# Optimization experiments

Measured on AMD Instinct MI355X. Metric: run time of the kernel, lower is better.

The kernel has to match this reference:

```python
import jax, jax.numpy as jnp
import numpy as np

VOCAB, EMB, HID, B, T = 50000, 300, 150, 256, 512

def _lstm_params(key, in_dim, hid):
    k1, k2, k3, k4 = jax.random.split(key, 4)
    s = 1.0 / np.sqrt(hid)
    return (jax.random.uniform(k1, (4 * hid, in_dim), minval=-s, maxval=s),
            jax.random.uniform(k2, (4 * hid, hid), minval=-s, maxval=s),
            jax.random.uniform(k3, (4 * hid,), minval=-s, maxval=s),
            jax.random.uniform(k4, (4 * hid,), minval=-s, maxval=s))

def setup_inputs() -> dict:
    key = jax.random.key(0)
    ks = jax.random.split(key, 16)
    emb = jax.random.normal(ks[0], (VOCAB, EMB), dtype=jnp.float32)
    emb = emb.at[0].set(0.0)  # padding_idx=0
    x = jax.random.randint(ks[1], (B, T), 0, VOCAB, dtype=jnp.int64)
    lengths = jax.random.randint(ks[2], (B,), 1, T + 1, dtype=jnp.int64)
    inp = {"x": x, "lengths": lengths, "emb": emb}
    in_dims = [EMB, HID, HID, HID]  # lstm1 layers 0,1 ; lstm2 layers 0,1
    for l in range(4):
        Wih, Whh, bih, bhh = _lstm_params(ks[3 + l], in_dims[l], HID)
        inp[f"Wih{l}"], inp[f"Whh{l}"], inp[f"bih{l}"], inp[f"bhh{l}"] = Wih, Whh, bih, bhh
    s = 1.0 / np.sqrt(HID)
    inp["fc1_w"] = jax.random.uniform(ks[8], (HID, HID), minval=-s, maxval=s)
    inp["fc1_b"] = jax.random.uniform(ks[9], (HID,), minval=-s, maxval=s)
    inp["fc2_w"] = jax.random.uniform(ks[10], (1, HID), minval=-s, maxval=s)
    inp["fc2_b"] = jax.random.uniform(ks[11], (1,), minval=-s, maxval=s)
    return inp

def _lstm_layer(x_seq, lengths, Wih, Whh, bih, bhh):
    # x_seq: [B, T, D]. Packed-sequence semantics: state updated only while t < length;
    # padded output positions are zero (matching pad_packed_sequence).
    Bsz, Tlen, _ = x_seq.shape
    hid = Whh.shape[1]
    x_proj = jnp.einsum('btd,gd->btg', x_seq, Wih) + bih + bhh  # [B,T,4H]

    def step(carry, inp):
        h, c = carry
        xg, t = inp
        gates = xg + h @ Whh.T
        i, f, g, o = jnp.split(gates, 4, axis=-1)
        i, f, o = jax.nn.sigmoid(i), jax.nn.sigmoid(f), jax.nn.sigmoid(o)
        g = jnp.tanh(g)
        c_new = f * c + i * g
        h_new = o * jnp.tanh(c_new)
        mask = (t < lengths)[:, None]
        h = jnp.where(mask, h_new, h)
        c = jnp.where(mask, c_new, c)
        out = jnp.where(mask, h_new, 0.0)
        return (h, c), out

    h0 = jnp.zeros((Bsz, hid), x_seq.dtype)
    (hT, cT), outs = jax.lax.scan(step, (h0, h0),
                                  (jnp.swapaxes(x_proj, 0, 1), jnp.arange(Tlen)))
    return jnp.swapaxes(outs, 0, 1), hT

def reference(x, lengths, emb,
              Wih0, Whh0, bih0, bhh0, Wih1, Whh1, bih1, bhh1,
              Wih2, Whh2, bih2, bhh2, Wih3, Whh3, bih3, bhh3,
              fc1_w, fc1_b, fc2_w, fc2_b):
    h = emb[x]  # [B, T, EMB] embedding lookup
    # lstm1 (2 layers)
    h, _ = _lstm_layer(h, lengths, Wih0, Whh0, bih0, bhh0)
    h, _ = _lstm_layer(h, lengths, Wih1, Whh1, bih1, bhh1)
    # lstm2 (2 layers); hn from its last layer
    h, _ = _lstm_layer(h, lengths, Wih2, Whh2, bih2, bhh2)
    _, hn = _lstm_layer(h, lengths, Wih3, Whh3, bih3, bhh3)
    z = jax.nn.relu(hn @ fc1_w.T + fc1_b)
    out = z @ fc2_w.T + fc2_b
    return out.flatten()
```

## Files before the change

kernel.cpp:

```cpp
#include <hip/hip_runtime.h>

#define HIDN 150
#define NG   600
#define NGP  640
#define TT   512
#define NBATCH 256
#define KPA  160
#define KPE  320

typedef __attribute__((ext_vector_type(8))) short bf16x8;
typedef __attribute__((ext_vector_type(4))) float f32x4;

__device__ __forceinline__ unsigned short f2bf(float v) {
    unsigned int u = __builtin_bit_cast(unsigned int, v);
    u += 0x7fffu + ((u >> 16) & 1u);
    return (unsigned short)(u >> 16);
}
__device__ __forceinline__ float bf2f(unsigned short h) {
    unsigned int u = ((unsigned int)h) << 16;
    return __builtin_bit_cast(float, u);
}

#define GLDS(gp, lp) __builtin_amdgcn_global_load_lds( \
    (const __attribute__((address_space(1))) unsigned int*)(gp), \
    (__attribute__((address_space(3))) unsigned int*)(lp), 16, 0, 0)

__global__ __launch_bounds__(256) void embprep_kernel(
    const float* __restrict__ emb,
    unsigned short* __restrict__ eh, unsigned short* __restrict__ el)
{
    int i = blockIdx.x * 256 + threadIdx.x;
    if (i >= 50000 * KPE) return;
    int v = i / KPE, k = i - v * KPE;
    float x = (k < 300) ? emb[(size_t)v * 300 + k] : 0.f;
    unsigned short hi = f2bf(x);
    eh[i] = hi;
    el[i] = f2bf(x - bf2f(hi));
}

__global__ __launch_bounds__(256) void prep_kernel(
    const float* __restrict__ Wih, const float* __restrict__ Whh,
    const float* __restrict__ bih, const float* __restrict__ bhh,
    int K, int Kp,
    unsigned short* __restrict__ Wgh, unsigned short* __restrict__ Wgl,
    float* __restrict__ Wts, float* __restrict__ bsum)
{
    int i = blockIdx.x * 256 + threadIdx.x;
    int nW = NGP * Kp;
    if (i < nW) {
        int n = i / Kp, k = i - n * Kp;
        float w = (n < NG && k < K) ? Wih[(size_t)n * K + k] : 0.f;
        unsigned short hi = f2bf(w);
        Wgh[i] = hi;
        Wgl[i] = f2bf(w - bf2f(hi));
    } else if (i < nW + HIDN * NGP) {
        int j = i - nW;
        int k = j / NGP, n = j - k * NGP;
        Wts[j] = (n < NG) ? Whh[(size_t)n * HIDN + k] : 0.f;
    } else if (i < nW + HIDN * NGP + NGP) {
        int g = i - nW - HIDN * NGP;
        bsum[g] = (g < NG) ? (bih[g] + bhh[g]) : 0.f;
    }
}

__global__ __launch_bounds__(256, 2) void gemm_kernel(
    const unsigned short* __restrict__ Ah, const unsigned short* __restrict__ Al,
    const int* __restrict__ gather,
    const unsigned short* __restrict__ Eh, const unsigned short* __restrict__ El,
    int Kp,
    const unsigned short* __restrict__ Wh, const unsigned short* __restrict__ Wl,
    const float* __restrict__ bsum, const int* __restrict__ lengths,
    float* __restrict__ G,
    int b_off, int t0, int lTc)
{
    int m0 = blockIdx.x * 128;
    int n0 = blockIdx.y * 128;
    int Tcm1 = (1 << lTc) - 1;
    if (lTc >= 7) {
        int b = b_off + (m0 >> lTc);
        if (t0 + (m0 & Tcm1) >= lengths[b]) return;
    }

    __shared__ __align__(16) unsigned short Ash[128][32];
    __shared__ __align__(16) unsigned short Asl[128][32];
    __shared__ __align__(16) unsigned short Bsh[128][32];
    __shared__ __align__(16) unsigned short Bsl[128][32];

    int tid = threadIdx.x, lane = tid & 63, wave = tid >> 6;

    const unsigned short* AhB = gather ? Eh : Ah;
    const unsigned short* AlB = gather ? El : Al;
    size_t ra[2], rb[2];
    int mrow[2];
    #pragma unroll
    for (int c2 = 0; c2 < 2; ++c2) {
        int mb = wave * 32 + c2 * 16;
        mrow[c2] = mb;
        int rg = m0 + mb + (lane >> 2);
        int bb = rg >> lTc, tl = rg & Tcm1;
        ra[c2] = gather ? (size_t)gather[(b_off + bb) * TT + t0 + tl] * (size_t)Kp
                        : ((size_t)bb * TT + t0 + tl) * (size_t)Kp;
        int nr = n0 + mb + (lane >> 2);
        rb[c2] = (size_t)nr * (size_t)Kp;
    }
    int klane = (lane & 3) * 8;

    f32x4 acc[4][4];
    #pragma unroll
    for (int i = 0; i < 4; ++i)
        #pragma unroll
        for (int j = 0; j < 4; ++j) acc[i][j] = (f32x4){0.f, 0.f, 0.f, 0.f};

    int fr = (lane >> 4) * 8;
    int ml = lane & 15;
    int mbase = (wave & 1) * 64;
    int nbase = (wave >> 1) * 64;

    for (int k0 = 0; k0 < Kp; k0 += 32) {
        #pragma unroll
        for (int c2 = 0; c2 < 2; ++c2) {
            GLDS(AhB + ra[c2] + k0 + klane, &Ash[mrow[c2]][0]);
            GLDS(AlB + ra[c2] + k0 + klane, &Asl[mrow[c2]][0]);
            GLDS(Wh  + rb[c2] + k0 + klane, &Bsh[mrow[c2]][0]);
            GLDS(Wl  + rb[c2] + k0 + klane, &Bsl[mrow[c2]][0]);
        }
        __syncthreads();

        bf16x8 afh[4], afl[4], bfh[4], bfl[4];
        #pragma unroll
        for (int i = 0; i < 4; ++i) {
            afh[i] = *(const bf16x8*)&Ash[mbase + i * 16 + ml][fr];
            afl[i] = *(const bf16x8*)&Asl[mbase + i * 16 + ml][fr];
            bfh[i] = *(const bf16x8*)&Bsh[nbase + i * 16 + ml][fr];
            bfl[i] = *(const bf16x8*)&Bsl[nbase + i * 16 + ml][fr];
        }
        #pragma unroll
        for (int i = 0; i < 4; ++i)
            #pragma unroll
            for (int j = 0; j < 4; ++j)
                acc[i][j] = __builtin_amdgcn_mfma_f32_16x16x32_bf16(afh[i], bfh[j], acc[i][j], 0, 0, 0);
        #pragma unroll
        for (int i = 0; i < 4; ++i)
            #pragma unroll
            for (int j = 0; j < 4; ++j)
                acc[i][j] = __builtin_amdgcn_mfma_f32_16x16x32_bf16(afh[i], bfl[j], acc[i][j], 0, 0, 0);
        #pragma unroll
        for (int i = 0; i < 4; ++i)
            #pragma unroll
            for (int j = 0; j < 4; ++j)
                acc[i][j] = __builtin_amdgcn_mfma_f32_16x16x32_bf16(afl[i], bfh[j], acc[i][j], 0, 0, 0);
        __syncthreads();
    }

    int rq = lane >> 4;
    #pragma unroll
    for (int i = 0; i < 4; ++i) {
        int mg = m0 + mbase + i * 16 + rq * 4;
        #pragma unroll
        for (int j = 0; j < 4; ++j) {
            int ng = n0 + nbase + j * 16 + ml;
            if (ng < NG) {
                float bz = bsum[ng];
                #pragma unroll
                for (int r = 0; r < 4; ++r)
                    G[(size_t)(mg + r) * NG + ng] = acc[i][j][r] + bz;
            }
        }
    }
}

#define REGK  32
#define TAILP 11

__global__ __launch_bounds__(640) void scan_kernel(
    const float* __restrict__ G,
    const float* __restrict__ Wt,
    const int*   __restrict__ lengths,
    unsigned short* __restrict__ Aout,
    unsigned short* __restrict__ Alout,
    float* __restrict__ hnb,
    float* __restrict__ hst, float* __restrict__ cst,
    int b_off, int t0, int Tc)
{
    __shared__ __align__(16) float h_s[152];
    __shared__ float gate_s[NG];
    __shared__ __align__(8) float wl2[TAILP][NGP][2];

    int tid = threadIdx.x;
    int l0 = blockIdx.x;
    int b  = b_off + l0;
    int len = lengths[b];
    int tmax = min(len, t0 + Tc);

    float4 wr[REGK];
    #pragma unroll
    for (int q = 0; q < REGK; ++q) {
        wr[q].x = Wt[(4 * q + 0) * NGP + tid];
        wr[q].y = Wt[(4 * q + 1) * NGP + tid];
        wr[q].z = Wt[(4 * q + 2) * NGP + tid];
        wr[q].w = Wt[(4 * q + 3) * NGP + tid];
    }
    #pragma unroll
    for (int p = 0; p < TAILP; ++p) {
        wl2[p][tid][0] = Wt[(128 + 2 * p) * NGP + tid];
        wl2[p][tid][1] = Wt[(129 + 2 * p) * NGP + tid];
    }

    float c = 0.f;
    if (tid < 152) h_s[tid] = 0.f;
    if (tid < HIDN && t0 > 0) {
        h_s[tid] = hst[l0 * HIDN + tid];
        c = cst[l0 * HIDN + tid];
    }

    bool isg    = (tid >= 2 * HIDN) && (tid < 3 * HIDN);
    bool act600 = (tid < NG);
    const float* Gbase = G + (size_t)l0 * Tc * NG + tid;
    __syncthreads();

    for (int t = t0; t < tmax; ++t) {
        float gval = act600 ? Gbase[(size_t)(t - t0) * NG] : 0.f;
        float acc = 0.f;
        #pragma unroll
        for (int q = 0; q < REGK; ++q) {
            float4 h4 = *(const float4*)&h_s[4 * q];
            acc += wr[q].x * h4.x; acc += wr[q].y * h4.y;
            acc += wr[q].z * h4.z; acc += wr[q].w * h4.w;
        }
        #pragma unroll
        for (int p = 0; p < TAILP; ++p) {
            float2 wp = *(const float2*)&wl2[p][tid][0];
            float2 hp = *(const float2*)&h_s[128 + 2 * p];
            acc += wp.x * hp.x; acc += wp.y * hp.y;
        }
        float a = gval + acc;
        float bb = isg ? 2.f * a : a;
        float e  = __expf(-bb);
        float r  = 1.f / (1.f + e);
        a = isg ? 2.f * r - 1.f : r;
        if (act600) gate_s[tid] = a;
        __syncthreads();
        if (tid < KPA) {
            float hv = 0.f;
            if (tid < HIDN) {
                float iv = gate_s[tid];
                float fv = gate_s[tid + HIDN];
                float gv = gate_s[tid + 2 * HIDN];
                float ov = gate_s[tid + 3 * HIDN];
                float cn = fv * c + iv * gv;
                float e2 = __expf(-2.f * cn);
                float th = 2.f / (1.f + e2) - 1.f;
                hv = ov * th;
                c = cn;
                h_s[tid] = hv;
                if (t == len - 1) hnb[b * HIDN + tid] = hv;
            }
            if (Aout) {
                size_t off = ((size_t)l0 * TT + t) * KPA + tid;
                unsigned short hi = f2bf(hv);
                Aout[off]  = hi;
                Alout[off] = f2bf(hv - bf2f(hi));
            }
        }
        __syncthreads();
    }

    if (tid < HIDN) {
        hst[l0 * HIDN + tid] = h_s[tid];
        cst[l0 * HIDN + tid] = c;
    }
}

__global__ __launch_bounds__(256) void head_kernel(
    const float* __restrict__ hnb, const float* __restrict__ fc1_w,
    const float* __restrict__ fc1_b, const float* __restrict__ fc2_w,
    const float* __restrict__ fc2_b, float* __restrict__ out)
{
    __shared__ float hs[HIDN];
    __shared__ float zs[HIDN];
    int b = blockIdx.x, tid = threadIdx.x;
    if (tid < HIDN) hs[tid] = hnb[b * HIDN + tid];
    __syncthreads();
    if (tid < HIDN) {
        float acc = fc1_b[tid];
        const float* wr = fc1_w + (size_t)tid * HIDN;
        #pragma unroll 5
        for (int k = 0; k < HIDN; ++k) acc += wr[k] * hs[k];
        zs[tid] = fmaxf(acc, 0.f);
    }
    __syncthreads();
    if (tid == 0) {
        float s = fc2_b[0];
        for (int k = 0; k < HIDN; ++k) s += fc2_w[k] * zs[k];
        out[b] = s;
    }
}

extern "C" void kernel_launch(void* const* d_in, const int* in_sizes, int n_in,
                              void* d_out, int out_size, void* d_ws, size_t ws_size,
                              hipStream_t stream)
{
    const int*   x       = (const int*)d_in[0];
    const int*   lengths = (const int*)d_in[1];
    const float* emb     = (const float*)d_in[2];
    const float *Wih[4], *Whh[4], *bih[4], *bhh[4];
    for (int l = 0; l < 4; ++l) {
        Wih[l] = (const float*)d_in[3 + 4 * l];
        Whh[l] = (const float*)d_in[4 + 4 * l];
        bih[l] = (const float*)d_in[5 + 4 * l];
        bhh[l] = (const float*)d_in[6 + 4 * l];
    }
    const float* fc1_w = (const float*)d_in[19];
    const float* fc1_b = (const float*)d_in[20];
    const float* fc2_w = (const float*)d_in[21];
    const float* fc2_b = (const float*)d_in[22];

    int Kl[4]  = {300, 150, 150, 150};
    int Kp[4]  = {KPE, KPA, KPA, KPA};
    size_t wgoff[4];
    size_t wgacc = 0;
    for (int l = 0; l < 4; ++l) { wgoff[l] = wgacc; wgacc += 2 * (size_t)NGP * Kp[l]; }

    size_t wf = ws_size / sizeof(float);
    const size_t WFIX = 384000 + 2560 + 38400 + 512000 + 16000000;
    int NBc = 0, Tc = 0;
    for (int nb = 256; nb >= 16; nb >>= 1) {
        for (int tc = 512; tc >= 8; tc >>= 1) {
            size_t need = WFIX + (size_t)nb * 300
                        + (size_t)nb * TT * (2 * KPA / 2)
                        + (size_t)nb * tc * NG;
            if (need <= wf) { NBc = nb; Tc = tc; break; }
        }
        if (NBc) break;
    }
    if (!NBc) return;
    int lTc = __builtin_ctz(Tc);

    float* ws  = (float*)d_ws;
    float* Wts = ws;
    float* bsm = Wts + 384000;
    float* hnb = bsm + 2560;
    unsigned short* Wg = (unsigned short*)(hnb + 38400);
    unsigned short* embh = Wg + 1024000;
    unsigned short* embl = embh + 16000000;
    float* hst = (float*)(embl + 16000000);
    float* cst = hst + (size_t)NBc * HIDN;
    unsigned short* Ahh = (unsigned short*)(cst + (size_t)NBc * HIDN);
    unsigned short* Ahl = Ahh + (size_t)NBc * TT * KPA;
    float* G   = (float*)(Ahl + (size_t)NBc * TT * KPA);

    embprep_kernel<<<(50000 * KPE + 255) / 256, 256, 0, stream>>>(emb, embh, embl);
    for (int l = 0; l < 4; ++l) {
        int total = NGP * Kp[l] + HIDN * NGP + NGP;
        prep_kernel<<<(total + 255) / 256, 256, 0, stream>>>(
            Wih[l], Whh[l], bih[l], bhh[l], Kl[l], Kp[l],
            Wg + wgoff[l], Wg + wgoff[l] + (size_t)NGP * Kp[l],
            Wts + l * 96000, bsm + l * 640);
    }

    int nTc = TT / Tc;
    int nBc = NBATCH / NBc;
    dim3 ggrid((unsigned)(NBc * Tc / 128), 5);
    for (int bc = 0; bc < nBc; ++bc) {
        int b_off = bc * NBc;
        for (int l = 0; l < 4; ++l) {
            const unsigned short* Wh = Wg + wgoff[l];
            const unsigned short* Wl = Wh + (size_t)NGP * Kp[l];
            for (int tc = 0; tc < nTc; ++tc) {
                int t0 = tc * Tc;
                gemm_kernel<<<ggrid, 256, 0, stream>>>(
                    (l == 0) ? nullptr : Ahh, (l == 0) ? nullptr : Ahl,
                    (l == 0) ? x : nullptr, embh, embl,
                    Kp[l], Wh, Wl, bsm + l * 640, lengths, G, b_off, t0, lTc);
                scan_kernel<<<NBc, 640, 0, stream>>>(
                    G, Wts + l * 96000, lengths,
                    (l == 3) ? nullptr : Ahh, (l == 3) ? nullptr : Ahl,
                    hnb, hst, cst, b_off, t0, Tc);
            }
        }
    }
    head_kernel<<<256, 256, 0, stream>>>(hnb, fc1_w, fc1_b, fc2_w, fc2_b, (float*)d_out);
}
```

Baseline: 3.364 ms.

## Interleave gate columns per wavefront and use shuffles to drop a scan barrier

Gate columns are permuted so that each 64-lane wavefront holds the i, f, g and o pre-activations for the same 16 hidden units. The GEMM writes G in this slot order and the recurrent weights are permuted to match. The cell update now gathers gates with lane shuffles instead of a shared gate buffer. Together with a double-buffered hidden state, this removes one block-wide barrier per timestep in the latency-bound recurrence, and the next step's G value is prefetched one step ahead. In exchange, the padded K columns 150–159 of the bf16 activation output are no longer written by the scan, and G grows to a padded 640-column stride.

```diff
diff --git a/kernel.cpp b/kernel.cpp
--- a/kernel.cpp
+++ b/kernel.cpp
@@ -24,6 +24,11 @@
 #define GLDS(gp, lp) __builtin_amdgcn_global_load_lds( \
     (const __attribute__((address_space(1))) unsigned int*)(gp), \
     (__attribute__((address_space(3))) unsigned int*)(lp), 16, 0, 0)
+
+__device__ __forceinline__ int slot_of(int n) {
+    int g = n / HIDN, u = n - g * HIDN;
+    return ((u >> 4) << 6) + (g << 4) + (u & 15);
+}
 
 __global__ __launch_bounds__(256) void embprep_kernel(
     const float* __restrict__ emb,
@@ -55,8 +60,10 @@
         Wgl[i] = f2bf(w - bf2f(hi));
     } else if (i < nW + HIDN * NGP) {
         int j = i - nW;
-        int k = j / NGP, n = j - k * NGP;
-        Wts[j] = (n < NG) ? Whh[(size_t)n * HIDN + k] : 0.f;
+        int k = j / NGP, s = j - k * NGP;
+        int u = ((s >> 6) << 4) + (s & 15);
+        int g = (s >> 4) & 3;
+        Wts[j] = (u < HIDN) ? Whh[(size_t)(g * HIDN + u) * HIDN + k] : 0.f;
     } else if (i < nW + HIDN * NGP + NGP) {
         int g = i - nW - HIDN * NGP;
         bsum[g] = (g < NG) ? (bih[g] + bhh[g]) : 0.f;
@@ -161,9 +168,10 @@
             int ng = n0 + nbase + j * 16 + ml;
             if (ng < NG) {
                 float bz = bsum[ng];
+                int s = slot_of(ng);
                 #pragma unroll
                 for (int r = 0; r < 4; ++r)
-                    G[(size_t)(mg + r) * NG + ng] = acc[i][j][r] + bz;
+                    G[(size_t)(mg + r) * NGP + s] = acc[i][j][r] + bz;
             }
         }
     }
@@ -182,11 +190,15 @@
     float* __restrict__ hst, float* __restrict__ cst,
     int b_off, int t0, int Tc)
 {
-    __shared__ __align__(16) float h_s[152];
-    __shared__ float gate_s[NG];
+    __shared__ __align__(16) float h_s[2][160];
     __shared__ __align__(8) float wl2[TAILP][NGP][2];
 
     int tid = threadIdx.x;
+    int lane = tid & 63, w = tid >> 6;
+    int u_loc = lane & 15, g = (lane >> 4) & 3;
+    int u = w * 16 + u_loc;
+    bool own = (lane < 16) && (u < HIDN);
+
     int l0 = blockIdx.x;
     int b  = b_off + l0;
     int len = lengths[b];
@@ -207,67 +219,63 @@
     }
 
     float c = 0.f;
-    if (tid < 152) h_s[tid] = 0.f;
-    if (tid < HIDN && t0 > 0) {
-        h_s[tid] = hst[l0 * HIDN + tid];
-        c = cst[l0 * HIDN + tid];
-    }
-
-    bool isg    = (tid >= 2 * HIDN) && (tid < 3 * HIDN);
-    bool act600 = (tid < NG);
-    const float* Gbase = G + (size_t)l0 * Tc * NG + tid;
+    if (tid < 160) { h_s[0][tid] = 0.f; h_s[1][tid] = 0.f; }
+    if (tid < HIDN && t0 > 0) h_s[0][tid] = hst[l0 * HIDN + tid];
+    if (own && t0 > 0) c = cst[l0 * HIDN + u];
+
+    bool isg = (g == 2);
+    const float* Gbase = G + (size_t)l0 * Tc * NGP + tid;
     __syncthreads();
 
+    int p = 0;
+    float gnext = (t0 < tmax) ? Gbase[(size_t)0] : 0.f;
     for (int t = t0; t < tmax; ++t) {
-        float gval = act600 ? Gbase[(size_t)(t - t0) * NG] : 0.f;
+        float gcur = gnext;
+        if (t + 1 < tmax) gnext = Gbase[(size_t)(t + 1 - t0) * NGP];
+        const float* hp = &h_s[p][0];
         float acc = 0.f;
         #pragma unroll
         for (int q = 0; q < REGK; ++q) {
-            float4 h4 = *(const float4*)&h_s[4 * q];
+            float4 h4 = *(const float4*)&hp[4 * q];
             acc += wr[q].x * h4.x; acc += wr[q].y * h4.y;
             acc += wr[q].z * h4.z; acc += wr[q].w * h4.w;
         }
         #pragma unroll
-        for (int p = 0; p < TAILP; ++p) {
-            float2 wp = *(const float2*)&wl2[p][tid][0];
-            float2 hp = *(const float2*)&h_s[128 + 2 * p];
-            acc += wp.x * hp.x; acc += wp.y * hp.y;
-        }
-        float a = gval + acc;
+        for (int q = 0; q < TAILP; ++q) {
+            float2 wp = *(const float2*)&wl2[q][tid][0];
+            float2 h2 = *(const float2*)&hp[128 + 2 * q];
+            acc += wp.x * h2.x; acc += wp.y * h2.y;
+        }
+        float a = gcur + acc;
         float bb = isg ? 2.f * a : a;
         float e  = __expf(-bb);
         float r  = 1.f / (1.f + e);
-        a = isg ? 2.f * r - 1.f : r;
-        if (act600) gate_s[tid] = a;
-        __syncthreads();
-        if (tid < KPA) {
-            float hv = 0.f;
-            if (tid < HIDN) {
-                float iv = gate_s[tid];
-                float fv = gate_s[tid + HIDN];
-                float gv = gate_s[tid + 2 * HIDN];
-                float ov = gate_s[tid + 3 * HIDN];
-                float cn = fv * c + iv * gv;
-                float e2 = __expf(-2.f * cn);
-                float th = 2.f / (1.f + e2) - 1.f;
-                hv = ov * th;
-                c = cn;
-                h_s[tid] = hv;
-                if (t == len - 1) hnb[b * HIDN + tid] = hv;
-            }
+        float av = isg ? 2.f * r - 1.f : r;
+        float fv = __shfl(av, u_loc + 16, 64);
+        float gv = __shfl(av, u_loc + 32, 64);
+        float ov = __shfl(av, u_loc + 48, 64);
+        if (own) {
+            float cn = fv * c + av * gv;
+            float e2 = __expf(-2.f * cn);
+            float th = 2.f / (1.f + e2) - 1.f;
+            float hv = ov * th;
+            c = cn;
+            h_s[p ^ 1][u] = hv;
             if (Aout) {
-                size_t off = ((size_t)l0 * TT + t) * KPA + tid;
+                size_t off = ((size_t)l0 * TT + t) * KPA + u;
                 unsigned short hi = f2bf(hv);
                 Aout[off]  = hi;
                 Alout[off] = f2bf(hv - bf2f(hi));
             }
+            if (t == len - 1) hnb[b * HIDN + u] = hv;
         }
         __syncthreads();
-    }
-
-    if (tid < HIDN) {
-        hst[l0 * HIDN + tid] = h_s[tid];
-        cst[l0 * HIDN + tid] = c;
+        p ^= 1;
+    }
+
+    if (own) {
+        hst[l0 * HIDN + u] = h_s[p][u];
+        cst[l0 * HIDN + u] = c;
     }
 }
 
@@ -327,8 +335,8 @@
     for (int nb = 256; nb >= 16; nb >>= 1) {
         for (int tc = 512; tc >= 8; tc >>= 1) {
             size_t need = WFIX + (size_t)nb * 300
-                        + (size_t)nb * TT * (2 * KPA / 2)
-                        + (size_t)nb * tc * NG;
+                        + (size_t)nb * TT * KPA
+                        + (size_t)nb * tc * NGP;
             if (need <= wf) { NBc = nb; Tc = tc; break; }
         }
         if (NBc) break;
```

Result: no change. 3.344 ms (-0.6%).

## Batch 16 sequences per scan block and use bf16x3 MFMA for recurrence

Applied to the files above, without the earlier changes.

The recurrent scan now handles 16 batch rows per block and computes h·Whh with split-bf16 (hi/lo) MFMA instructions, with the weights held in registers. Before, each block ran one sequence with scalar FP32 FMAs. The G slab for the next step is prefetched into LDS with async global_load_lds double buffering, and the gemm's row ordering is interleaved so each 16-row tile is 16 sequences at one timestep, with G padded to 640 columns. This cuts the number of scan blocks by 16x and moves the serial matvec onto matrix cores. In exchange, a step runs until the longest of the 16 sequences ends, precision falls to roughly three-term bf16 emulation, and there are only 16 blocks, so fewer CUs are used.

```diff
diff --git a/kernel.cpp b/kernel.cpp
--- a/kernel.cpp
+++ b/kernel.cpp
@@ -38,29 +38,25 @@
     el[i] = f2bf(x - bf2f(hi));
 }
 
-__global__ __launch_bounds__(256) void prep_kernel(
-    const float* __restrict__ Wih, const float* __restrict__ Whh,
+__global__ __launch_bounds__(256) void split_kernel(
+    const float* __restrict__ src, int K, int Kp,
+    unsigned short* __restrict__ dh, unsigned short* __restrict__ dl)
+{
+    int i = blockIdx.x * 256 + threadIdx.x;
+    if (i >= NGP * Kp) return;
+    int n = i / Kp, k = i - n * Kp;
+    float w = (n < NG && k < K) ? src[(size_t)n * K + k] : 0.f;
+    unsigned short hi = f2bf(w);
+    dh[i] = hi;
+    dl[i] = f2bf(w - bf2f(hi));
+}
+
+__global__ __launch_bounds__(256) void bias_kernel(
     const float* __restrict__ bih, const float* __restrict__ bhh,
-    int K, int Kp,
-    unsigned short* __restrict__ Wgh, unsigned short* __restrict__ Wgl,
-    float* __restrict__ Wts, float* __restrict__ bsum)
-{
-    int i = blockIdx.x * 256 + threadIdx.x;
-    int nW = NGP * Kp;
-    if (i < nW) {
-        int n = i / Kp, k = i - n * Kp;
-        float w = (n < NG && k < K) ? Wih[(size_t)n * K + k] : 0.f;
-        unsigned short hi = f2bf(w);
-        Wgh[i] = hi;
-        Wgl[i] = f2bf(w - bf2f(hi));
-    } else if (i < nW + HIDN * NGP) {
-        int j = i - nW;
-        int k = j / NGP, n = j - k * NGP;
-        Wts[j] = (n < NG) ? Whh[(size_t)n * HIDN + k] : 0.f;
-    } else if (i < nW + HIDN * NGP + NGP) {
-        int g = i - nW - HIDN * NGP;
-        bsum[g] = (g < NG) ? (bih[g] + bhh[g]) : 0.f;
-    }
+    float* __restrict__ bsum)
+{
+    int g = blockIdx.x * 256 + threadIdx.x;
+    if (g < NGP) bsum[g] = (g < NG) ? (bih[g] + bhh[g]) : 0.f;
 }
 
 __global__ __launch_bounds__(256, 2) void gemm_kernel(
@@ -75,10 +71,13 @@
 {
     int m0 = blockIdx.x * 128;
     int n0 = blockIdx.y * 128;
-    int Tcm1 = (1 << lTc) - 1;
-    if (lTc >= 7) {
-        int b = b_off + (m0 >> lTc);
-        if (t0 + (m0 & Tcm1) >= lengths[b]) return;
+    int grpm = (1 << (lTc + 4)) - 1;
+    {
+        int bg = m0 >> (lTc + 4);
+        int tl0 = (m0 & grpm) >> 4;
+        int bm = 0;
+        for (int i = 0; i < 16; ++i) bm = max(bm, lengths[b_off + bg * 16 + i]);
+        if (t0 + tl0 >= bm) return;
     }
 
     __shared__ __align__(16) unsigned short Ash[128][32];
@@ -97,9 +96,12 @@
         int mb = wave * 32 + c2 * 16;
         mrow[c2] = mb;
         int rg = m0 + mb + (lane >> 2);
-        int bb = rg >> lTc, tl = rg & Tcm1;
-        ra[c2] = gather ? (size_t)gather[(b_off + bb) * TT + t0 + tl] * (size_t)Kp
-                        : ((size_t)bb * TT + t0 + tl) * (size_t)Kp;
+        int bg = rg >> (lTc + 4);
+        int r2 = rg & grpm;
+        int tl = r2 >> 4, m16 = r2 & 15;
+        int bl = bg * 16 + m16;
+        ra[c2] = gather ? (size_t)gather[(b_off + bl) * TT + t0 + tl] * (size_t)Kp
+                        : ((size_t)bl * TT + t0 + tl) * (size_t)Kp;
         int nr = n0 + mb + (lane >> 2);
         rb[c2] = (size_t)nr * (size_t)Kp;
     }
@@ -159,115 +161,175 @@
         #pragma unroll
         for (int j = 0; j < 4; ++j) {
             int ng = n0 + nbase + j * 16 + ml;
-            if (ng < NG) {
-                float bz = bsum[ng];
-                #pragma unroll
-                for (int r = 0; r < 4; ++r)
-                    G[(size_t)(mg + r) * NG + ng] = acc[i][j][r] + bz;
-            }
-        }
-    }
-}
-
-#define REGK  32
-#define TAILP 11
-
-__global__ __launch_bounds__(640) void scan_kernel(
+            float bz = bsum[ng];
+            #pragma unroll
+            for (int r = 0; r < 4; ++r)
+                G[(size_t)(mg + r) * NGP + ng] = acc[i][j][r] + bz;
+        }
+    }
+}
+
+#define GS(g, u, m) (((g) * 151 + (u)) * 17 + (m))
+
+__global__ __launch_bounds__(512, 2) void scan_kernel(
     const float* __restrict__ G,
-    const float* __restrict__ Wt,
-    const int*   __restrict__ lengths,
-    unsigned short* __restrict__ Aout,
-    unsigned short* __restrict__ Alout,
+    const unsigned short* __restrict__ Whs, const unsigned short* __restrict__ Wls,
+    const int* __restrict__ lengths,
+    unsigned short* __restrict__ Aout, unsigned short* __restrict__ Alout,
     float* __restrict__ hnb,
     float* __restrict__ hst, float* __restrict__ cst,
     int b_off, int t0, int Tc)
 {
-    __shared__ __align__(16) float h_s[152];
-    __shared__ float gate_s[NG];
-    __shared__ __align__(8) float wl2[TAILP][NGP][2];
+    __shared__ __align__(16) float Gbuf[2][16 * NGP];
+    __shared__ float gate_s[4 * 151 * 17];
+    __shared__ __align__(16) unsigned short h_hi[16][168];
+    __shared__ __align__(16) unsigned short h_lo[16][168];
+    __shared__ int len_s[16];
 
     int tid = threadIdx.x;
-    int l0 = blockIdx.x;
-    int b  = b_off + l0;
-    int len = lengths[b];
-    int tmax = min(len, t0 + Tc);
-
-    float4 wr[REGK];
-    #pragma unroll
-    for (int q = 0; q < REGK; ++q) {
-        wr[q].x = Wt[(4 * q + 0) * NGP + tid];
-        wr[q].y = Wt[(4 * q + 1) * NGP + tid];
-        wr[q].z = Wt[(4 * q + 2) * NGP + tid];
-        wr[q].w = Wt[(4 * q + 3) * NGP + tid];
-    }
-    #pragma unroll
-    for (int p = 0; p < TAILP; ++p) {
-        wl2[p][tid][0] = Wt[(128 + 2 * p) * NGP + tid];
-        wl2[p][tid][1] = Wt[(129 + 2 * p) * NGP + tid];
-    }
-
-    float c = 0.f;
-    if (tid < 152) h_s[tid] = 0.f;
-    if (tid < HIDN && t0 > 0) {
-        h_s[tid] = hst[l0 * HIDN + tid];
-        c = cst[l0 * HIDN + tid];
-    }
-
-    bool isg    = (tid >= 2 * HIDN) && (tid < 3 * HIDN);
-    bool act600 = (tid < NG);
-    const float* Gbase = G + (size_t)l0 * Tc * NG + tid;
+    int lane = tid & 63, w = tid >> 6;
+    int ml = lane & 15, quad = lane >> 4;
+    int fr = quad * 8;
+    int bl16 = blockIdx.x * 16;
+    int bB = b_off + bl16;
+
+    bf16x8 Bh[5][5], Bl[5][5];
+    #pragma unroll
+    for (int q = 0; q < 5; ++q) {
+        int ncol = w * 80 + q * 16 + ml;
+        #pragma unroll
+        for (int ks = 0; ks < 5; ++ks) {
+            Bh[q][ks] = *(const bf16x8*)&Whs[(size_t)ncol * KPA + ks * 32 + fr];
+            Bl[q][ks] = *(const bf16x8*)&Wls[(size_t)ncol * KPA + ks * 32 + fr];
+        }
+    }
+
+    if (tid < 16) len_s[tid] = lengths[bB + tid];
+    for (int i = tid; i < 16 * 168; i += 512) {
+        h_hi[0][i] = 0; h_lo[0][i] = 0;
+    }
+
+    float creg[5], hreg[5];
+    #pragma unroll
+    for (int p = 0; p < 5; ++p) { creg[p] = 0.f; hreg[p] = 0.f; }
+    if (t0 > 0) {
+        #pragma unroll
+        for (int p = 0; p < 5; ++p) {
+            int pi = tid + 512 * p;
+            if (pi < 16 * HIDN) {
+                int m = pi / HIDN, u = pi - m * HIDN;
+                hreg[p] = hst[(bl16 + m) * HIDN + u];
+                creg[p] = cst[(bl16 + m) * HIDN + u];
+            }
+        }
+    }
     __syncthreads();
+    if (t0 > 0) {
+        #pragma unroll
+        for (int p = 0; p < 5; ++p) {
+            int pi = tid + 512 * p;
+            if (pi < 16 * HIDN) {
+                int m = pi / HIDN, u = pi - m * HIDN;
+                unsigned short hi = f2bf(hreg[p]);
+                h_hi[m][u] = hi;
+                h_lo[m][u] = f2bf(hreg[p] - bf2f(hi));
+            }
+        }
+    }
+
+    int bm = 0;
+    for (int i = 0; i < 16; ++i) bm = max(bm, len_s[i]);
+    int tmax = min(bm, t0 + Tc);
+
+    const float* Gblk = G + (size_t)blockIdx.x * Tc * (16 * NGP);
+    #define STAGE(bufi, tl) do { \
+        const float* slab_ = Gblk + (size_t)(tl) * (16 * NGP); \
+        _Pragma("unroll") \
+        for (int i_ = 0; i_ < 5; ++i_) \
+            GLDS(slab_ + i_ * 2048 + w * 256 + lane * 4, &Gbuf[bufi][i_ * 2048 + w * 256]); \
+    } while (0)
+
+    if (t0 < tmax) STAGE(0, 0);
+    __syncthreads();
 
     for (int t = t0; t < tmax; ++t) {
-        float gval = act600 ? Gbase[(size_t)(t - t0) * NG] : 0.f;
-        float acc = 0.f;
-        #pragma unroll
-        for (int q = 0; q < REGK; ++q) {
-            float4 h4 = *(const float4*)&h_s[4 * q];
-            acc += wr[q].x * h4.x; acc += wr[q].y * h4.y;
-            acc += wr[q].z * h4.z; acc += wr[q].w * h4.w;
-        }
-        #pragma unroll
-        for (int p = 0; p < TAILP; ++p) {
-            float2 wp = *(const float2*)&wl2[p][tid][0];
-            float2 hp = *(const float2*)&h_s[128 + 2 * p];
-            acc += wp.x * hp.x; acc += wp.y * hp.y;
-        }
-        float a = gval + acc;
-        float bb = isg ? 2.f * a : a;
-        float e  = __expf(-bb);
-        float r  = 1.f / (1.f + e);
-        a = isg ? 2.f * r - 1.f : r;
-        if (act600) gate_s[tid] = a;
+        int tl = t - t0;
+        int buf = tl & 1;
+        if (t + 1 < tmax) STAGE(buf ^ 1, tl + 1);
+
+        f32x4 acc[5];
+        #pragma unroll
+        for (int q = 0; q < 5; ++q) acc[q] = (f32x4){0.f, 0.f, 0.f, 0.f};
+        #pragma unroll
+        for (int ks = 0; ks < 5; ++ks) {
+            bf16x8 ah = *(const bf16x8*)&h_hi[ml][ks * 32 + fr];
+            bf16x8 al = *(const bf16x8*)&h_lo[ml][ks * 32 + fr];
+            #pragma unroll
+            for (int q = 0; q < 5; ++q) {
+                acc[q] = __builtin_amdgcn_mfma_f32_16x16x32_bf16(ah, Bh[q][ks], acc[q], 0, 0, 0);
+                acc[q] = __builtin_amdgcn_mfma_f32_16x16x32_bf16(ah, Bl[q][ks], acc[q], 0, 0, 0);
+                acc[q] = __builtin_amdgcn_mfma_f32_16x16x32_bf16(al, Bh[q][ks], acc[q], 0, 0, 0);
+            }
+        }
+        #pragma unroll
+        for (int q = 0; q < 5; ++q) {
+            int ncol = w * 80 + q * 16 + ml;
+            if (ncol < NG) {
+                int g = ncol / HIDN, u = ncol - g * HIDN;
+                bool isg = (g == 2);
+                #pragma unroll
+                for (int r = 0; r < 4; ++r) {
+                    int m = quad * 4 + r;
+                    float a = acc[q][r] + Gbuf[buf][m * NGP + ncol];
+                    float bb = isg ? 2.f * a : a;
+                    float e  = __expf(-bb);
+                    float rr = 1.f / (1.f + e);
+                    gate_s[GS(g, u, m)] = isg ? 2.f * rr - 1.f : rr;
+                }
+            }
+        }
         __syncthreads();
-        if (tid < KPA) {
-            float hv = 0.f;
-            if (tid < HIDN) {
-                float iv = gate_s[tid];
-                float fv = gate_s[tid + HIDN];
-                float gv = gate_s[tid + 2 * HIDN];
-                float ov = gate_s[tid + 3 * HIDN];
-                float cn = fv * c + iv * gv;
+
+        #pragma unroll
+        for (int p = 0; p < 5; ++p) {
+            int pi = tid + 512 * p;
+            if (pi < 16 * HIDN) {
+                int m = pi / HIDN, u = pi - m * HIDN;
+                float iv = gate_s[GS(0, u, m)];
+                float fv = gate_s[GS(1, u, m)];
+                float gv = gate_s[GS(2, u, m)];
+                float ov = gate_s[GS(3, u, m)];
+                float cn = fv * creg[p] + iv * gv;
                 float e2 = __expf(-2.f * cn);
                 float th = 2.f / (1.f + e2) - 1.f;
-                hv = ov * th;
-                c = cn;
-                h_s[tid] = hv;
-                if (t == len - 1) hnb[b * HIDN + tid] = hv;
-            }
-            if (Aout) {
-                size_t off = ((size_t)l0 * TT + t) * KPA + tid;
+                float hv = ov * th;
+                int ln = len_s[m];
+                bool upd = (t < ln);
                 unsigned short hi = f2bf(hv);
-                Aout[off]  = hi;
-                Alout[off] = f2bf(hv - bf2f(hi));
+                unsigned short lo = f2bf(hv - bf2f(hi));
+                if (upd) {
+                    creg[p] = cn; hreg[p] = hv;
+                    h_hi[m][u] = hi; h_lo[m][u] = lo;
+                }
+                if (Aout) {
+                    size_t off = ((size_t)(bl16 + m) * TT + t) * KPA + u;
+                    Aout[off]  = upd ? hi : (unsigned short)0;
+                    Alout[off] = upd ? lo : (unsigned short)0;
+                }
+                if (t == ln - 1) hnb[(bB + m) * HIDN + u] = hv;
             }
         }
         __syncthreads();
     }
 
-    if (tid < HIDN) {
-        hst[l0 * HIDN + tid] = h_s[tid];
-        cst[l0 * HIDN + tid] = c;
+    #pragma unroll
+    for (int p = 0; p < 5; ++p) {
+        int pi = tid + 512 * p;
+        if (pi < 16 * HIDN) {
+            int m = pi / HIDN, u = pi - m * HIDN;
+            hst[(bl16 + m) * HIDN + u] = hreg[p];
+            cst[(bl16 + m) * HIDN + u] = creg[p];
+        }
     }
 }
 
@@ -315,20 +377,19 @@
     const float* fc2_w = (const float*)d_in[21];
     const float* fc2_b = (const float*)d_in[22];
 
-    int Kl[4]  = {300, 150, 150, 150};
-    int Kp[4]  = {KPE, KPA, KPA, KPA};
-    size_t wgoff[4];
-    size_t wgacc = 0;
-    for (int l = 0; l < 4; ++l) { wgoff[l] = wgacc; wgacc += 2 * (size_t)NGP * Kp[l]; }
+    int Kl[4] = {300, 150, 150, 150};
+    int Kp[4] = {KPE, KPA, KPA, KPA};
+    size_t wioff[4], wiacc = 0;
+    for (int l = 0; l < 4; ++l) { wioff[l] = wiacc; wiacc += 2 * (size_t)NGP * Kp[l]; }
 
     size_t wf = ws_size / sizeof(float);
-    const size_t WFIX = 384000 + 2560 + 38400 + 512000 + 16000000;
+    const size_t WFIX = 2560 + 38400 + 512000 + 409600 + 16000000;
     int NBc = 0, Tc = 0;
     for (int nb = 256; nb >= 16; nb >>= 1) {
         for (int tc = 512; tc >= 8; tc >>= 1) {
             size_t need = WFIX + (size_t)nb * 300
-                        + (size_t)nb * TT * (2 * KPA / 2)
-                        + (size_t)nb * tc * NG;
+                        + (size_t)nb * TT * (KPA / 2) * 2
+                        + (size_t)nb * tc * NGP;
             if (need <= wf) { NBc = nb; Tc = tc; break; }
         }
         if (NBc) break;
@@ -337,11 +398,11 @@
     int lTc = __builtin_ctz(Tc);
 
     float* ws  = (float*)d_ws;
-    float* Wts = ws;
-    float* bsm = Wts + 384000;
+    float* bsm = ws;
     float* hnb = bsm + 2560;
-    unsigned short* Wg = (unsigned short*)(hnb + 38400);
-    unsigned short* embh = Wg + 1024000;
+    unsigned short* WgI = (unsigned short*)(hnb + 38400);
+    unsigned short* WgH = WgI + 1024000;
+    unsigned short* embh = WgH + 819200;
     unsigned short* embl = embh + 16000000;
     float* hst = (float*)(embl + 16000000);
     float* cst = hst + (size_t)NBc * HIDN;
@@ -351,11 +412,12 @@
 
     embprep_kernel<<<(50000 * KPE + 255) / 256, 256, 0, stream>>>(emb, embh, embl);
     for (int l = 0; l < 4; ++l) {
-        int total = NGP * Kp[l] + HIDN * NGP + NGP;
-        prep_kernel<<<(total + 255) / 256, 256, 0, stream>>>(
-            Wih[l], Whh[l], bih[l], bhh[l], Kl[l], Kp[l],
-            Wg + wgoff[l], Wg + wgoff[l] + (size_t)NGP * Kp[l],
-            Wts + l * 96000, bsm + l * 640);
+        split_kernel<<<(NGP * Kp[l] + 255) / 256, 256, 0, stream>>>(
+            Wih[l], Kl[l], Kp[l], WgI + wioff[l], WgI + wioff[l] + (size_t)NGP * Kp[l]);
+        split_kernel<<<(NGP * KPA + 255) / 256, 256, 0, stream>>>(
+            Whh[l], HIDN, KPA,
+            WgH + (size_t)l * 2 * NGP * KPA, WgH + (size_t)l * 2 * NGP * KPA + NGP * KPA);
+        bias_kernel<<<3, 256, 0, stream>>>(bih[l], bhh[l], bsm + l * 640);
     }
 
     int nTc = TT / Tc;
@@ -364,16 +426,18 @@
     for (int bc = 0; bc < nBc; ++bc) {
         int b_off = bc * NBc;
         for (int l = 0; l < 4; ++l) {
-            const unsigned short* Wh = Wg + wgoff[l];
-            const unsigned short* Wl = Wh + (size_t)NGP * Kp[l];
+            const unsigned short* WhI = WgI + wioff[l];
+            const unsigned short* WlI = WhI + (size_t)NGP * Kp[l];
+            const unsigned short* WhH = WgH + (size_t)l * 2 * NGP * KPA;
+            const unsigned short* WlH = WhH + (size_t)NGP * KPA;
             for (int tc = 0; tc < nTc; ++tc) {
                 int t0 = tc * Tc;
                 gemm_kernel<<<ggrid, 256, 0, stream>>>(
                     (l == 0) ? nullptr : Ahh, (l == 0) ? nullptr : Ahl,
                     (l == 0) ? x : nullptr, embh, embl,
-                    Kp[l], Wh, Wl, bsm + l * 640, lengths, G, b_off, t0, lTc);
-                scan_kernel<<<NBc, 640, 0, stream>>>(
-                    G, Wts + l * 96000, lengths,
+                    Kp[l], WhI, WlI, bsm + l * 640, lengths, G, b_off, t0, lTc);
+                scan_kernel<<<NBc / 16, 512, 0, stream>>>(
+                    G, WhH, WlH, lengths,
                     (l == 3) ? nullptr : Ahh, (l == 3) ? nullptr : Ahl,
                     hnb, hst, cst, b_off, t0, Tc);
             }
```

Result: slower. 13.27 ms (+294.5%).
